# Performance work log

Measured on AMD Instinct MI355X. Metric: run time of the kernel, lower is better.

The kernel has to match this reference:

```python
import jax, jax.numpy as jnp
import numpy as np

N_NODES = 100000
N_EDGES = 1600000
N_GRAPHS = 64
IN_DIM = 128
HIDDEN = 64
OUT_DIM = 6


def gcn_conv(x, W, b, src, dst, n_nodes):
    """PyG GCNConv: D^{-1/2} (A + I) D^{-1/2} X W + b (self-loops added)."""
    xw = x @ W  # [N, H]
    # degree including self-loop (computed over destination nodes)
    deg = jax.ops.segment_sum(jnp.ones((src.shape[0],), xw.dtype), dst,
                              num_segments=n_nodes) + 1.0
    dinv = jax.lax.rsqrt(deg)  # deg >= 1, always safe
    # per-edge normalized messages, scatter-add into destinations
    coef = (dinv[src] * dinv[dst])[:, None]  # [E, 1]
    agg = jax.ops.segment_sum(xw[src] * coef, dst, num_segments=n_nodes)
    # self-loop contribution: dinv[i]^2 * xw[i]
    agg = agg + xw * (dinv * dinv)[:, None]
    return agg + b


def setup_inputs() -> dict:
    key = jax.random.key(0)
    ks = jax.random.split(key, 9)
    x = jax.random.normal(ks[0], (N_NODES, IN_DIM), dtype=jnp.float32)
    edge_index = jax.random.randint(ks[1], (2, N_EDGES), 0, N_NODES, dtype=jnp.int64)
    batch = jnp.sort(jax.random.randint(ks[2], (N_NODES,), 0, N_GRAPHS, dtype=jnp.int64))
    # Glorot-ish params
    W1 = jax.random.normal(ks[3], (IN_DIM, HIDDEN), dtype=jnp.float32) / np.sqrt(IN_DIM)
    b1 = jnp.zeros((HIDDEN,), jnp.float32)
    W2 = jax.random.normal(ks[4], (HIDDEN, HIDDEN), dtype=jnp.float32) / np.sqrt(HIDDEN)
    b2 = jnp.zeros((HIDDEN,), jnp.float32)
    Wl = jax.random.normal(ks[5], (HIDDEN, OUT_DIM), dtype=jnp.float32) / np.sqrt(HIDDEN)
    bl = jnp.zeros((OUT_DIM,), jnp.float32)
    return {"x": x, "edge_index": edge_index, "batch": batch,
            "W1": W1, "b1": b1, "W2": W2, "b2": b2, "Wl": Wl, "bl": bl}


def reference(x, edge_index, batch, W1, b1, W2, b2, Wl, bl):
    src, dst = edge_index[0], edge_index[1]
    h = jax.nn.relu(gcn_conv(x, W1, b1, src, dst, N_NODES))
    # dropout is identity in eval mode
    h = gcn_conv(h, W2, b2, src, dst, N_NODES)
    # global mean pool over graph ids
    sums = jax.ops.segment_sum(h, batch, num_segments=N_GRAPHS)  # [G, H]
    cnts = jax.ops.segment_sum(jnp.ones((h.shape[0],), h.dtype), batch,
                               num_segments=N_GRAPHS)
    pooled = sums / jnp.maximum(cnts, 1.0)[:, None]
    return pooled @ Wl + bl  # [G, OUT_DIM]
```

## Files before the change

kernel.cpp:

```cpp
#include <hip/hip_runtime.h>

#define NCOL 64
#define BSH 8
#define NBMAX 512
#define EPB 2048
#define P2CAP 6144
#define NREP 8

typedef __attribute__((ext_vector_type(8))) short bf16x8;
typedef __attribute__((ext_vector_type(4))) float f32x4;


__device__ __forceinline__ float bf_lo(unsigned int v) { return __uint_as_float(v << 16); }
__device__ __forceinline__ float bf_hi(unsigned int v) { return __uint_as_float(v & 0xFFFF0000u); }
__device__ __forceinline__ unsigned short bfs(float x) {
  unsigned int u = __float_as_uint(x);
  u = (u + 0x7FFFu + ((u >> 16) & 1u)) >> 16;
  return (unsigned short)u;
}


__global__ __launch_bounds__(256) void bin_p1(const int* __restrict__ src,
                                              const int* __restrict__ dst,
                                              unsigned int* __restrict__ ent,
                                              int* __restrict__ blockOff,
                                              int ne, int nb) {
  __shared__ int hist[NBMAX];
  __shared__ int base[NBMAX];
  __shared__ int part[256];
  __shared__ unsigned int stage[EPB];
  int tid = threadIdx.x;
  int e0 = blockIdx.x * EPB;
  int cnt = min(EPB, ne - e0);

  for (int i = tid; i < NBMAX; i += 256) hist[i] = 0;
  __syncthreads();
  for (int i = tid; i < cnt; i += 256) {
    int d = dst[e0 + i];
    atomicAdd(&hist[d >> BSH], 1);
  }
  __syncthreads();

  int a0 = hist[2 * tid], a1 = hist[2 * tid + 1];
  int s = a0 + a1;
  part[tid] = s;
  __syncthreads();
  for (int d = 1; d < 256; d <<= 1) {
    int v = (tid >= d) ? part[tid - d] : 0;
    __syncthreads();
    part[tid] += v;
    __syncthreads();
  }
  int off = part[tid] - s;
  base[2 * tid] = off;
  base[2 * tid + 1] = off + a0;
  __syncthreads();

  for (int b = tid; b < nb; b += 256) blockOff[(size_t)blockIdx.x * nb + b] = base[b];
  for (int i = tid; i < NBMAX; i += 256) hist[i] = base[i];
  __syncthreads();

  for (int i = tid; i < cnt; i += 256) {
    int d = dst[e0 + i];
    int sv = src[e0 + i];
    unsigned int e = ((unsigned int)(d & ((1 << BSH) - 1)) << 17) | (unsigned int)sv;
    int p = atomicAdd(&hist[d >> BSH], 1);
    stage[p] = e;
  }
  __syncthreads();
  for (int i = tid; i < cnt; i += 256) ent[e0 + i] = stage[i];
}


__global__ __launch_bounds__(256) void deg_bin(const unsigned int* __restrict__ ent,
                                               const int* __restrict__ blockOff,
                                               int* __restrict__ degi,
                                               int n, int ne, int nb, int nblk) {
  __shared__ int cnt[256];
  int b = blockIdx.x;
  int tid = threadIdx.x;
  cnt[tid] = 0;
  __syncthreads();
  for (int blk = tid; blk < nblk; blk += 256) {
    int e0 = blk * EPB;
    int bcnt = min(EPB, ne - e0);
    int st = blockOff[(size_t)blk * nb + b];
    int en = (b + 1 < nb) ? blockOff[(size_t)blk * nb + b + 1] : bcnt;
    for (int i = st; i < en; ++i) {
      unsigned int e = ent[e0 + i];
      atomicAdd(&cnt[e >> 17], 1);
    }
  }
  __syncthreads();
  int node = (b << BSH) + tid;
  if (node < n) degi[node] = cnt[tid];
}

__global__ void dinv_kernel(const int* __restrict__ degi, float* __restrict__ dinv, int n) {
  int i = blockIdx.x * blockDim.x + threadIdx.x;
  if (i < n) dinv[i] = rsqrtf((float)degi[i] + 1.0f);
}


__global__ void bounds_kernel(const int* __restrict__ batch, int* __restrict__ startg,
                              int* __restrict__ endg, int n) {
  int i = blockIdx.x * blockDim.x + threadIdx.x;
  if (i >= n) return;
  int b = batch[i];
  if (i == 0) {
    startg[b] = 0;
  } else {
    int bp = batch[i - 1];
    if (b != bp) { startg[b] = i; endg[bp] = i; }
  }
  if (i == n - 1) endg[b] = n;
}


#define SCAN_C 8

__global__ void scan_part(const int* __restrict__ degi, int* __restrict__ tsum,
                          int n, int nthreads) {
  int t = blockIdx.x * blockDim.x + threadIdx.x;
  if (t >= nthreads) return;
  int lo = t * SCAN_C, hi = min(lo + SCAN_C, n);
  int s = 0;
  for (int i = lo; i < hi; ++i) s += degi[i];
  tsum[t] = s;
}

__global__ void scan_mid(int* __restrict__ tsum, int* __restrict__ toff, int nthreads) {
  __shared__ int part[1024];
  int t = threadIdx.x;
  int chunk = (nthreads + 1023) >> 10;
  int lo = t * chunk, hi = min(lo + chunk, nthreads);
  int s = 0;
  for (int i = lo; i < hi; ++i) s += tsum[i];
  part[t] = s;
  __syncthreads();
  for (int d = 1; d < 1024; d <<= 1) {
    int v = (t >= d) ? part[t - d] : 0;
    __syncthreads();
    part[t] += v;
    __syncthreads();
  }
  int off = part[t] - s;
  for (int i = lo; i < hi; ++i) { toff[i] = off; off += tsum[i]; }
}

__global__ void scan_fill(const int* __restrict__ degi, const int* __restrict__ toff,
                          int* __restrict__ rowptr, int n, int nthreads) {
  int t = blockIdx.x * blockDim.x + threadIdx.x;
  if (t >= nthreads) return;
  int lo = t * SCAN_C, hi = min(lo + SCAN_C, n);
  int off = toff[t];
  for (int i = lo; i < hi; ++i) {
    rowptr[i] = off;
    off += degi[i];
  }
  if (hi == n) rowptr[n] = off;
}


__global__ __launch_bounds__(256) void bin_p2(const unsigned int* __restrict__ ent,
                                              const int* __restrict__ blockOff,
                                              const int* __restrict__ rowptr,
                                              int* __restrict__ csr_src,
                                              int n, int ne, int nb, int nblk) {
  __shared__ int cur[256];
  __shared__ int outS[P2CAP];
  int b = blockIdx.x;
  int tid = threadIdx.x;
  int node0 = b << BSH;
  int node1 = min(node0 + 256, n);
  int bucketBase = rowptr[node0];
  int bucketCnt = rowptr[node1] - bucketBase;
  int node = node0 + tid;
  cur[tid] = (node < node1) ? (rowptr[node] - bucketBase) : 0;
  __syncthreads();
  for (int blk = tid; blk < nblk; blk += 256) {
    int e0 = blk * EPB;
    int bcnt = min(EPB, ne - e0);
    int st = blockOff[(size_t)blk * nb + b];
    int en = (b + 1 < nb) ? blockOff[(size_t)blk * nb + b + 1] : bcnt;
    for (int i = st; i < en; ++i) {
      unsigned int e = ent[e0 + i];
      int dL = e >> 17;
      int sv = (int)(e & 0x1FFFFu);
      int p = atomicAdd(&cur[dL], 1);
      if (p < P2CAP) outS[p] = sv;
      else csr_src[bucketBase + p] = sv;
    }
  }
  __syncthreads();
  int lim = min(bucketCnt, P2CAP);
  for (int i = tid; i < lim; i += 256) csr_src[bucketBase + i] = outS[i];
}


template<int K>
__global__ __launch_bounds__(256, 8) void gemm_mfma(
    const float* __restrict__ X, const float* __restrict__ W,
    const float* __restrict__ dinv, unsigned int* __restrict__ Ybf, int n) {
  __shared__ unsigned short YS[64][64];
  int tid = threadIdx.x;
  int w = tid >> 6;
  int l = tid & 63;
  int lr = l & 15;
  int lk = l >> 4;
  int rows0 = blockIdx.x * 64;

  bf16x8 bfrag[K / 32];
#pragma unroll
  for (int s = 0; s < K / 32; ++s) {
#pragma unroll
    for (int j = 0; j < 8; ++j) {
      int k = s * 32 + lk * 8 + j;
      bfrag[s][j] = (short)bfs(W[(size_t)k * NCOL + 16 * w + lr]);
    }
  }

  f32x4 acc[4];
#pragma unroll
  for (int rt = 0; rt < 4; ++rt) acc[rt] = (f32x4){0.f, 0.f, 0.f, 0.f};

#pragma unroll
  for (int rt = 0; rt < 4; ++rt) {
    int row = min(rows0 + rt * 16 + lr, n - 1);
    const float* xr = X + (size_t)row * K + lk * 8;
#pragma unroll
    for (int s = 0; s < K / 32; ++s) {
      float4 x0 = *reinterpret_cast<const float4*>(xr + s * 32);
      float4 x1 = *reinterpret_cast<const float4*>(xr + s * 32 + 4);
      bf16x8 af;
      af[0] = (short)bfs(x0.x); af[1] = (short)bfs(x0.y);
      af[2] = (short)bfs(x0.z); af[3] = (short)bfs(x0.w);
      af[4] = (short)bfs(x1.x); af[5] = (short)bfs(x1.y);
      af[6] = (short)bfs(x1.z); af[7] = (short)bfs(x1.w);
      acc[rt] = __builtin_amdgcn_mfma_f32_16x16x32_bf16(af, bfrag[s], acc[rt], 0, 0, 0);
    }
  }

#pragma unroll
  for (int rt = 0; rt < 4; ++rt) {
#pragma unroll
    for (int j = 0; j < 4; ++j) {
      int row = rt * 16 + lk * 4 + j;
      float d = dinv[min(rows0 + row, n - 1)];
      YS[row][16 * w + lr] = bfs(acc[rt][j] * d);
    }
  }
  __syncthreads();

  const uint4* ys4 = reinterpret_cast<const uint4*>(&YS[0][0]);
  for (int idx = tid; idx < 512; idx += 256) {
    int row = idx >> 3;
    int gr = rows0 + row;
    if (gr < n)
      reinterpret_cast<uint4*>(Ybf + (size_t)gr * 32)[idx & 7] = ys4[idx];
  }
}


__global__ __launch_bounds__(256) void aggregate_relu(
    const int* __restrict__ rowptr, const int* __restrict__ csr_src,
    const uint4* __restrict__ Ybf4, const float* __restrict__ dinv,
    const float* __restrict__ bias, float* __restrict__ H, int n) {
  int nd = (blockIdx.x * blockDim.x + threadIdx.x) >> 3;
  if (nd >= n) return;
  int l = threadIdx.x & 7;
  int lo = rowptr[nd], hi = rowptr[nd + 1];

  uint4 vs = Ybf4[(size_t)nd * 8 + l];
  float a0 = bf_lo(vs.x), a1 = bf_hi(vs.x);
  float a2 = bf_lo(vs.y), a3 = bf_hi(vs.y);
  float a4 = bf_lo(vs.z), a5 = bf_hi(vs.z);
  float a6 = bf_lo(vs.w), a7 = bf_hi(vs.w);

  int p = lo;
  for (; p + 3 < hi; p += 4) {
    int s0 = csr_src[p];
    int s1 = csr_src[p + 1];
    int s2 = csr_src[p + 2];
    int s3 = csr_src[p + 3];
    uint4 v0 = Ybf4[(size_t)s0 * 8 + l];
    uint4 v1 = Ybf4[(size_t)s1 * 8 + l];
    uint4 v2 = Ybf4[(size_t)s2 * 8 + l];
    uint4 v3 = Ybf4[(size_t)s3 * 8 + l];
    a0 += bf_lo(v0.x); a1 += bf_hi(v0.x);
    a2 += bf_lo(v0.y); a3 += bf_hi(v0.y);
    a4 += bf_lo(v0.z); a5 += bf_hi(v0.z);
    a6 += bf_lo(v0.w); a7 += bf_hi(v0.w);
    a0 += bf_lo(v1.x); a1 += bf_hi(v1.x);
    a2 += bf_lo(v1.y); a3 += bf_hi(v1.y);
    a4 += bf_lo(v1.z); a5 += bf_hi(v1.z);
    a6 += bf_lo(v1.w); a7 += bf_hi(v1.w);
    a0 += bf_lo(v2.x); a1 += bf_hi(v2.x);
    a2 += bf_lo(v2.y); a3 += bf_hi(v2.y);
    a4 += bf_lo(v2.z); a5 += bf_hi(v2.z);
    a6 += bf_lo(v2.w); a7 += bf_hi(v2.w);
    a0 += bf_lo(v3.x); a1 += bf_hi(v3.x);
    a2 += bf_lo(v3.y); a3 += bf_hi(v3.y);
    a4 += bf_lo(v3.z); a5 += bf_hi(v3.z);
    a6 += bf_lo(v3.w); a7 += bf_hi(v3.w);
  }
  for (; p < hi; ++p) {
    int s = csr_src[p];
    uint4 v = Ybf4[(size_t)s * 8 + l];
    a0 += bf_lo(v.x); a1 += bf_hi(v.x);
    a2 += bf_lo(v.y); a3 += bf_hi(v.y);
    a4 += bf_lo(v.z); a5 += bf_hi(v.z);
    a6 += bf_lo(v.w); a7 += bf_hi(v.w);
  }

  float d = dinv[nd];
  float4 b0 = *reinterpret_cast<const float4*>(bias + l * 8);
  float4 b1 = *reinterpret_cast<const float4*>(bias + l * 8 + 4);
  float4 o0, o1;
  o0.x = fmaf(d, a0, b0.x); o0.y = fmaf(d, a1, b0.y);
  o0.z = fmaf(d, a2, b0.z); o0.w = fmaf(d, a3, b0.w);
  o1.x = fmaf(d, a4, b1.x); o1.y = fmaf(d, a5, b1.y);
  o1.z = fmaf(d, a6, b1.z); o1.w = fmaf(d, a7, b1.w);
  o0.x = fmaxf(o0.x, 0.f); o0.y = fmaxf(o0.y, 0.f);
  o0.z = fmaxf(o0.z, 0.f); o0.w = fmaxf(o0.w, 0.f);
  o1.x = fmaxf(o1.x, 0.f); o1.y = fmaxf(o1.y, 0.f);
  o1.z = fmaxf(o1.z, 0.f); o1.w = fmaxf(o1.w, 0.f);
  float* hr = H + (size_t)nd * NCOL + l * 8;
  *reinterpret_cast<float4*>(hr) = o0;
  *reinterpret_cast<float4*>(hr + 4) = o1;
}


__global__ __launch_bounds__(256) void aggregate_pool(
    const int* __restrict__ rowptr, const int* __restrict__ csr_src,
    const uint4* __restrict__ Ybf4, const float* __restrict__ dinv,
    const float* __restrict__ bias, const int* __restrict__ batch,
    float* __restrict__ poolrep, int n) {
  __shared__ float poolS[4][64];
  __shared__ int gS[4];
  __shared__ int uniS[4];
  int tid = threadIdx.x;
  int nd = (blockIdx.x * blockDim.x + tid) >> 3;
  int w = tid >> 6;
  int l = tid & 7;
  bool active = nd < n;
  int ndc = active ? nd : (n - 1);
  int lo = rowptr[ndc];
  int hi = active ? rowptr[ndc + 1] : lo;

  uint4 vs = Ybf4[(size_t)ndc * 8 + l];
  float a0 = bf_lo(vs.x), a1 = bf_hi(vs.x);
  float a2 = bf_lo(vs.y), a3 = bf_hi(vs.y);
  float a4 = bf_lo(vs.z), a5 = bf_hi(vs.z);
  float a6 = bf_lo(vs.w), a7 = bf_hi(vs.w);

  int p = lo;
  for (; p + 3 < hi; p += 4) {
    int s0 = csr_src[p];
    int s1 = csr_src[p + 1];
    int s2 = csr_src[p + 2];
    int s3 = csr_src[p + 3];
    uint4 v0 = Ybf4[(size_t)s0 * 8 + l];
    uint4 v1 = Ybf4[(size_t)s1 * 8 + l];
    uint4 v2 = Ybf4[(size_t)s2 * 8 + l];
    uint4 v3 = Ybf4[(size_t)s3 * 8 + l];
    a0 += bf_lo(v0.x); a1 += bf_hi(v0.x);
    a2 += bf_lo(v0.y); a3 += bf_hi(v0.y);
    a4 += bf_lo(v0.z); a5 += bf_hi(v0.z);
    a6 += bf_lo(v0.w); a7 += bf_hi(v0.w);
    a0 += bf_lo(v1.x); a1 += bf_hi(v1.x);
    a2 += bf_lo(v1.y); a3 += bf_hi(v1.y);
    a4 += bf_lo(v1.z); a5 += bf_hi(v1.z);
    a6 += bf_lo(v1.w); a7 += bf_hi(v1.w);
    a0 += bf_lo(v2.x); a1 += bf_hi(v2.x);
    a2 += bf_lo(v2.y); a3 += bf_hi(v2.y);
    a4 += bf_lo(v2.z); a5 += bf_hi(v2.z);
    a6 += bf_lo(v2.w); a7 += bf_hi(v2.w);
    a0 += bf_lo(v3.x); a1 += bf_hi(v3.x);
    a2 += bf_lo(v3.y); a3 += bf_hi(v3.y);
    a4 += bf_lo(v3.z); a5 += bf_hi(v3.z);
    a6 += bf_lo(v3.w); a7 += bf_hi(v3.w);
  }
  for (; p < hi; ++p) {
    int s = csr_src[p];
    uint4 v = Ybf4[(size_t)s * 8 + l];
    a0 += bf_lo(v.x); a1 += bf_hi(v.x);
    a2 += bf_lo(v.y); a3 += bf_hi(v.y);
    a4 += bf_lo(v.z); a5 += bf_hi(v.z);
    a6 += bf_lo(v.w); a7 += bf_hi(v.w);
  }

  float d = dinv[ndc];
  float4 b0 = *reinterpret_cast<const float4*>(bias + l * 8);
  float4 b1 = *reinterpret_cast<const float4*>(bias + l * 8 + 4);
  float4 o0, o1;
  o0.x = fmaf(d, a0, b0.x); o0.y = fmaf(d, a1, b0.y);
  o0.z = fmaf(d, a2, b0.z); o0.w = fmaf(d, a3, b0.w);
  o1.x = fmaf(d, a4, b1.x); o1.y = fmaf(d, a5, b1.y);
  o1.z = fmaf(d, a6, b1.z); o1.w = fmaf(d, a7, b1.w);

  float* rep = poolrep + (size_t)(blockIdx.x & (NREP - 1)) * 4096;
  int gg = active ? batch[nd] : -1;
  int waveFirstNd = (blockIdx.x * blockDim.x + (tid & ~63)) >> 3;
  bool full = (waveFirstNd + 8 <= n);
  int g0 = __builtin_amdgcn_readfirstlane(gg);
  bool uni = full && __all(gg == g0);

  if (uni) {
#pragma unroll
    for (int m = 8; m < 64; m <<= 1) {
      o0.x += __shfl_xor(o0.x, m); o0.y += __shfl_xor(o0.y, m);
      o0.z += __shfl_xor(o0.z, m); o0.w += __shfl_xor(o0.w, m);
      o1.x += __shfl_xor(o1.x, m); o1.y += __shfl_xor(o1.y, m);
      o1.z += __shfl_xor(o1.z, m); o1.w += __shfl_xor(o1.w, m);
    }
    if ((tid & 63) < 8) {
      *reinterpret_cast<float4*>(&poolS[w][l * 8]) = o0;
      *reinterpret_cast<float4*>(&poolS[w][l * 8 + 4]) = o1;
    }
    if ((tid & 63) == 0) { gS[w] = g0; uniS[w] = 1; }
  } else {
    if ((tid & 63) == 0) { gS[w] = -1; uniS[w] = 0; }
    if (active) {
      float* pr = rep + (size_t)gg * NCOL + l * 8;
      atomicAdd(pr + 0, o0.x); atomicAdd(pr + 1, o0.y);
      atomicAdd(pr + 2, o0.z); atomicAdd(pr + 3, o0.w);
      atomicAdd(pr + 4, o1.x); atomicAdd(pr + 5, o1.y);
      atomicAdd(pr + 6, o1.z); atomicAdd(pr + 7, o1.w);
    }
  }
  __syncthreads();

  if (tid < 64) {
    bool bu = uniS[0] && uniS[1] && uniS[2] && uniS[3] &&
              gS[0] == gS[1] && gS[1] == gS[2] && gS[2] == gS[3];
    if (bu) {
      float s = poolS[0][tid] + poolS[1][tid] + poolS[2][tid] + poolS[3][tid];
      atomicAdd(&rep[(size_t)gS[0] * NCOL + tid], s);
    } else {
#pragma unroll
      for (int ww = 0; ww < 4; ++ww)
        if (uniS[ww]) atomicAdd(&rep[(size_t)gS[ww] * NCOL + tid], poolS[ww][tid]);
    }
  }
}


__global__ void final_kernel(const float* __restrict__ poolrep,
                             const int* __restrict__ startg,
                             const int* __restrict__ endg, const float* __restrict__ Wl,
                             const float* __restrict__ bl, float* __restrict__ out, int ng) {
  __shared__ float poolL[4096];
  int t = threadIdx.x;
  for (int idx = t; idx < ng * NCOL; idx += blockDim.x) {
    float s = 0.f;
#pragma unroll
    for (int r = 0; r < NREP; ++r) s += poolrep[(size_t)r * 4096 + idx];
    poolL[idx] = s;
  }
  __syncthreads();
  if (t >= ng * 6) return;
  int g = t / 6, o = t % 6;
  float cntf = (float)(endg[g] - startg[g]);
  float inv = 1.0f / fmaxf(cntf, 1.0f);
  float s = 0.f;
#pragma unroll
  for (int c = 0; c < NCOL; ++c) s += poolL[g * NCOL + c] * Wl[c * 6 + o];
  out[t] = fmaf(s, inv, bl[o]);
}


extern "C" void kernel_launch(void* const* d_in, const int* in_sizes, int n_in,
                              void* d_out, int out_size, void* d_ws, size_t ws_size,
                              hipStream_t stream) {
  const float* x    = (const float*)d_in[0];
  const int*   ei   = (const int*)d_in[1];
  const int*   batch= (const int*)d_in[2];
  const float* W1   = (const float*)d_in[3];
  const float* b1   = (const float*)d_in[4];
  const float* W2   = (const float*)d_in[5];
  const float* b2   = (const float*)d_in[6];
  const float* Wl   = (const float*)d_in[7];
  const float* bl   = (const float*)d_in[8];
  float* out = (float*)d_out;

  int n  = in_sizes[0] / 128;
  int ne = in_sizes[1] / 2;
  int ng = out_size / 6;
  const int* srcI = ei;
  const int* dstI = ei + ne;

  int nb   = (n + 255) >> BSH;
  int nblk = (ne + EPB - 1) / EPB;

  char* w = (char*)d_ws;
  size_t o = 0;
  auto take = [&](size_t bytes) -> char* {
    char* p = w + o;
    o = (o + bytes + 255) & ~(size_t)255;
    return p;
  };
  float*        dinv    = (float*)take((size_t)n * 4);
  int*          degi    = (int*)  take((size_t)n * 4);
  int*          rowptr  = (int*)  take((size_t)(n + 1) * 4);
  int*          csr_src = (int*)  take((size_t)ne * 4);
  unsigned int* ent     = (unsigned int*)take((size_t)ne * 4);
  int*          blockOff= (int*)  take((size_t)nblk * nb * 4);
  unsigned int* Ybf     = (unsigned int*)take((size_t)n * (NCOL / 2) * 4);
  float*        H       = (float*)take((size_t)n * NCOL * 4);
  float*        poolrep = (float*)take((size_t)NREP * 4096 * 4);
  int*          startg  = (int*)  take(64 * 4);
  int*          endg    = (int*)  take(64 * 4);
  int*          tsum    = (int*)  take(16384 * 4);
  int*          toff    = (int*)  take(16384 * 4);

  hipMemsetAsync(poolrep, 0, (size_t)NREP * 4096 * 4, stream);
  hipMemsetAsync(startg, 0, 64 * 4, stream);
  hipMemsetAsync(endg, 0, 64 * 4, stream);

  int nb256 = (n + 255) / 256;
  int nthreads = (n + SCAN_C - 1) / SCAN_C;
  int nbScan = (nthreads + 255) / 256;

  bin_p1<<<nblk, 256, 0, stream>>>(srcI, dstI, ent, blockOff, ne, nb);
  deg_bin<<<nb, 256, 0, stream>>>(ent, blockOff, degi, n, ne, nb, nblk);
  bounds_kernel<<<nb256, 256, 0, stream>>>(batch, startg, endg, n);
  dinv_kernel<<<nb256, 256, 0, stream>>>(degi, dinv, n);
  scan_part<<<nbScan, 256, 0, stream>>>(degi, tsum, n, nthreads);
  scan_mid<<<1, 1024, 0, stream>>>(tsum, toff, nthreads);
  scan_fill<<<nbScan, 256, 0, stream>>>(degi, toff, rowptr, n, nthreads);
  bin_p2<<<nb, 256, 0, stream>>>(ent, blockOff, rowptr, csr_src, n, ne, nb, nblk);

  int nbAgg = (n * 8 + 255) / 256;
  int nbGemm = (n + 63) / 64;

  gemm_mfma<128><<<nbGemm, 256, 0, stream>>>(x, W1, dinv, Ybf, n);
  aggregate_relu<<<nbAgg, 256, 0, stream>>>(rowptr, csr_src, (const uint4*)Ybf,
                                            dinv, b1, H, n);

  gemm_mfma<64><<<nbGemm, 256, 0, stream>>>(H, W2, dinv, Ybf, n);
  aggregate_pool<<<nbAgg, 256, 0, stream>>>(rowptr, csr_src, (const uint4*)Ybf,
                                            dinv, b2, batch, poolrep, n);

  final_kernel<<<1, 384, 0, stream>>>(poolrep, startg, endg, Wl, bl, out, ng);
}
```

Measured before the change: 211.9 us.

## Globally sort edge entries by destination bucket before degree and CSR passes

Replaces the per-block local binning with a global two-pass counting sort: a histogram kernel, a bucket-major prefix scan over (bucket, block) counts, then a scatter that writes each block's bucket slices to global sorted offsets. Degree counting and CSR fill then read one contiguous range per bucket with all threads striding over it, instead of each thread serially walking a per-block slice. This is meant to remove the uncoalesced, load-imbalanced per-thread serial loops in deg_bin/bin_p2. In exchange it adds an extra pass over dst, three scan kernels with integer divisions, and a scatter whose per-bucket copy loop is serial per thread and poorly coalesced.

```diff
diff --git a/kernel.cpp b/kernel.cpp
--- a/kernel.cpp
+++ b/kernel.cpp
@@ -6,6 +6,8 @@
 #define EPB 2048
 #define P2CAP 6144
 #define NREP 8
+#define SCAN_C 8
+#define SCAN2_C 16
 
 typedef __attribute__((ext_vector_type(8))) short bf16x8;
 typedef __attribute__((ext_vector_type(4))) float f32x4;
@@ -20,25 +22,86 @@
 }
 
 
-__global__ __launch_bounds__(256) void bin_p1(const int* __restrict__ src,
-                                              const int* __restrict__ dst,
-                                              unsigned int* __restrict__ ent,
-                                              int* __restrict__ blockOff,
-                                              int ne, int nb) {
+__global__ __launch_bounds__(256) void hist_p1(const int* __restrict__ dst,
+                                               int* __restrict__ blockOffC,
+                                               int ne, int nb) {
+  __shared__ int hist[NBMAX];
+  int tid = threadIdx.x;
+  int e0 = blockIdx.x * EPB;
+  int cnt = min(EPB, ne - e0);
+  for (int i = tid; i < NBMAX; i += 256) hist[i] = 0;
+  __syncthreads();
+  for (int i = tid; i < cnt; i += 256) atomicAdd(&hist[dst[e0 + i] >> BSH], 1);
+  __syncthreads();
+  for (int b = tid; b < nb; b += 256) blockOffC[(size_t)blockIdx.x * nb + b] = hist[b];
+}
+
+
+__global__ void scan2_part(const int* __restrict__ blockOffC, int* __restrict__ tsum,
+                           int total, int nthreads, int nblk, int nb) {
+  int t = blockIdx.x * blockDim.x + threadIdx.x;
+  if (t >= nthreads) return;
+  int lo = t * SCAN2_C, hi = min(lo + SCAN2_C, total);
+  int s = 0;
+  for (int f = lo; f < hi; ++f) {
+    int b = f / nblk, blk = f - b * nblk;
+    s += blockOffC[(size_t)blk * nb + b];
+  }
+  tsum[t] = s;
+}
+
+__global__ void scan_mid(int* __restrict__ tsum, int* __restrict__ toff, int nthreads) {
+  __shared__ int part[1024];
+  int t = threadIdx.x;
+  int chunk = (nthreads + 1023) >> 10;
+  int lo = t * chunk, hi = min(lo + chunk, nthreads);
+  int s = 0;
+  for (int i = lo; i < hi; ++i) s += tsum[i];
+  part[t] = s;
+  __syncthreads();
+  for (int d = 1; d < 1024; d <<= 1) {
+    int v = (t >= d) ? part[t - d] : 0;
+    __syncthreads();
+    part[t] += v;
+    __syncthreads();
+  }
+  int off = part[t] - s;
+  for (int i = lo; i < hi; ++i) { toff[i] = off; off += tsum[i]; }
+}
+
+__global__ void scan2_fill(const int* __restrict__ blockOffC, const int* __restrict__ toff,
+                           int* __restrict__ sortOff, int total, int nthreads,
+                           int nblk, int nb) {
+  int t = blockIdx.x * blockDim.x + threadIdx.x;
+  if (t >= nthreads) return;
+  int lo = t * SCAN2_C, hi = min(lo + SCAN2_C, total);
+  int off = toff[t];
+  for (int f = lo; f < hi; ++f) {
+    int b = f / nblk, blk = f - b * nblk;
+    sortOff[f] = off;
+    off += blockOffC[(size_t)blk * nb + b];
+  }
+}
+
+
+__global__ __launch_bounds__(256) void scatter_p1(const int* __restrict__ src,
+                                                  const int* __restrict__ dst,
+                                                  const int* __restrict__ sortOff,
+                                                  unsigned int* __restrict__ ent,
+                                                  int ne, int nb, int nblk) {
   __shared__ int hist[NBMAX];
   __shared__ int base[NBMAX];
+  __shared__ int cntL[NBMAX];
   __shared__ int part[256];
   __shared__ unsigned int stage[EPB];
   int tid = threadIdx.x;
-  int e0 = blockIdx.x * EPB;
+  int blk = blockIdx.x;
+  int e0 = blk * EPB;
   int cnt = min(EPB, ne - e0);
 
   for (int i = tid; i < NBMAX; i += 256) hist[i] = 0;
   __syncthreads();
-  for (int i = tid; i < cnt; i += 256) {
-    int d = dst[e0 + i];
-    atomicAdd(&hist[d >> BSH], 1);
-  }
+  for (int i = tid; i < cnt; i += 256) atomicAdd(&hist[dst[e0 + i] >> BSH], 1);
   __syncthreads();
 
   int a0 = hist[2 * tid], a1 = hist[2 * tid + 1];
@@ -52,11 +115,9 @@
     __syncthreads();
   }
   int off = part[tid] - s;
-  base[2 * tid] = off;
-  base[2 * tid + 1] = off + a0;
-  __syncthreads();
-
-  for (int b = tid; b < nb; b += 256) blockOff[(size_t)blockIdx.x * nb + b] = base[b];
+  base[2 * tid] = off;      cntL[2 * tid] = a0;
+  base[2 * tid + 1] = off + a0; cntL[2 * tid + 1] = a1;
+  __syncthreads();
   for (int i = tid; i < NBMAX; i += 256) hist[i] = base[i];
   __syncthreads();
 
@@ -68,29 +129,29 @@
     stage[p] = e;
   }
   __syncthreads();
-  for (int i = tid; i < cnt; i += 256) ent[e0 + i] = stage[i];
-}
-
-
-__global__ __launch_bounds__(256) void deg_bin(const unsigned int* __restrict__ ent,
-                                               const int* __restrict__ blockOff,
-                                               int* __restrict__ degi,
-                                               int n, int ne, int nb, int nblk) {
+
+  for (int b = tid; b < nb; b += 256) {
+    int c = cntL[b];
+    if (!c) continue;
+    int s0 = base[b];
+    int d0 = sortOff[(size_t)b * nblk + blk];
+    for (int i = 0; i < c; ++i) ent[d0 + i] = stage[s0 + i];
+  }
+}
+
+
+__global__ __launch_bounds__(256) void deg_sorted(const unsigned int* __restrict__ ent,
+                                                  const int* __restrict__ sortOff,
+                                                  int* __restrict__ degi,
+                                                  int n, int ne, int nb, int nblk) {
   __shared__ int cnt[256];
   int b = blockIdx.x;
   int tid = threadIdx.x;
   cnt[tid] = 0;
   __syncthreads();
-  for (int blk = tid; blk < nblk; blk += 256) {
-    int e0 = blk * EPB;
-    int bcnt = min(EPB, ne - e0);
-    int st = blockOff[(size_t)blk * nb + b];
-    int en = (b + 1 < nb) ? blockOff[(size_t)blk * nb + b + 1] : bcnt;
-    for (int i = st; i < en; ++i) {
-      unsigned int e = ent[e0 + i];
-      atomicAdd(&cnt[e >> 17], 1);
-    }
-  }
+  int st = sortOff[(size_t)b * nblk];
+  int en = (b + 1 < nb) ? sortOff[(size_t)(b + 1) * nblk] : ne;
+  for (int i = st + tid; i < en; i += 256) atomicAdd(&cnt[ent[i] >> 17], 1);
   __syncthreads();
   int node = (b << BSH) + tid;
   if (node < n) degi[node] = cnt[tid];
@@ -117,8 +178,6 @@
 }
 
 
-#define SCAN_C 8
-
 __global__ void scan_part(const int* __restrict__ degi, int* __restrict__ tsum,
                           int n, int nthreads) {
   int t = blockIdx.x * blockDim.x + threadIdx.x;
@@ -127,25 +186,6 @@
   int s = 0;
   for (int i = lo; i < hi; ++i) s += degi[i];
   tsum[t] = s;
-}
-
-__global__ void scan_mid(int* __restrict__ tsum, int* __restrict__ toff, int nthreads) {
-  __shared__ int part[1024];
-  int t = threadIdx.x;
-  int chunk = (nthreads + 1023) >> 10;
-  int lo = t * chunk, hi = min(lo + chunk, nthreads);
-  int s = 0;
-  for (int i = lo; i < hi; ++i) s += tsum[i];
-  part[t] = s;
-  __syncthreads();
-  for (int d = 1; d < 1024; d <<= 1) {
-    int v = (t >= d) ? part[t - d] : 0;
-    __syncthreads();
-    part[t] += v;
-    __syncthreads();
-  }
-  int off = part[t] - s;
-  for (int i = lo; i < hi; ++i) { toff[i] = off; off += tsum[i]; }
 }
 
 __global__ void scan_fill(const int* __restrict__ degi, const int* __restrict__ toff,
@@ -162,11 +202,11 @@
 }
 
 
-__global__ __launch_bounds__(256) void bin_p2(const unsigned int* __restrict__ ent,
-                                              const int* __restrict__ blockOff,
-                                              const int* __restrict__ rowptr,
-                                              int* __restrict__ csr_src,
-                                              int n, int ne, int nb, int nblk) {
+__global__ __launch_bounds__(256) void p2_sorted(const unsigned int* __restrict__ ent,
+                                                 const int* __restrict__ sortOff,
+                                                 const int* __restrict__ rowptr,
+                                                 int* __restrict__ csr_src,
+                                                 int n, int ne, int nb, int nblk) {
   __shared__ int cur[256];
   __shared__ int outS[P2CAP];
   int b = blockIdx.x;
@@ -178,19 +218,15 @@
   int node = node0 + tid;
   cur[tid] = (node < node1) ? (rowptr[node] - bucketBase) : 0;
   __syncthreads();
-  for (int blk = tid; blk < nblk; blk += 256) {
-    int e0 = blk * EPB;
-    int bcnt = min(EPB, ne - e0);
-    int st = blockOff[(size_t)blk * nb + b];
-    int en = (b + 1 < nb) ? blockOff[(size_t)blk * nb + b + 1] : bcnt;
-    for (int i = st; i < en; ++i) {
-      unsigned int e = ent[e0 + i];
-      int dL = e >> 17;
-      int sv = (int)(e & 0x1FFFFu);
-      int p = atomicAdd(&cur[dL], 1);
-      if (p < P2CAP) outS[p] = sv;
-      else csr_src[bucketBase + p] = sv;
-    }
+  int st = sortOff[(size_t)b * nblk];
+  int en = (b + 1 < nb) ? sortOff[(size_t)(b + 1) * nblk] : ne;
+  for (int i = st + tid; i < en; i += 256) {
+    unsigned int e = ent[i];
+    int dL = e >> 17;
+    int sv = (int)(e & 0x1FFFFu);
+    int p = atomicAdd(&cur[dL], 1);
+    if (p < P2CAP) outS[p] = sv;
+    else csr_src[bucketBase + p] = sv;
   }
   __syncthreads();
   int lim = min(bucketCnt, P2CAP);
@@ -492,6 +528,7 @@
 
   int nb   = (n + 255) >> BSH;
   int nblk = (ne + EPB - 1) / EPB;
+  int total2 = nb * nblk;
 
   char* w = (char*)d_ws;
   size_t o = 0;
@@ -500,19 +537,20 @@
     o = (o + bytes + 255) & ~(size_t)255;
     return p;
   };
-  float*        dinv    = (float*)take((size_t)n * 4);
-  int*          degi    = (int*)  take((size_t)n * 4);
-  int*          rowptr  = (int*)  take((size_t)(n + 1) * 4);
-  int*          csr_src = (int*)  take((size_t)ne * 4);
-  unsigned int* ent     = (unsigned int*)take((size_t)ne * 4);
-  int*          blockOff= (int*)  take((size_t)nblk * nb * 4);
-  unsigned int* Ybf     = (unsigned int*)take((size_t)n * (NCOL / 2) * 4);
-  float*        H       = (float*)take((size_t)n * NCOL * 4);
-  float*        poolrep = (float*)take((size_t)NREP * 4096 * 4);
-  int*          startg  = (int*)  take(64 * 4);
-  int*          endg    = (int*)  take(64 * 4);
-  int*          tsum    = (int*)  take(16384 * 4);
-  int*          toff    = (int*)  take(16384 * 4);
+  float*        dinv     = (float*)take((size_t)n * 4);
+  int*          degi     = (int*)  take((size_t)n * 4);
+  int*          rowptr   = (int*)  take((size_t)(n + 1) * 4);
+  int*          csr_src  = (int*)  take((size_t)ne * 4);
+  unsigned int* ent      = (unsigned int*)take((size_t)ne * 4);
+  int*          blockOffC= (int*)  take((size_t)total2 * 4);
+  int*          sortOff  = (int*)  take((size_t)total2 * 4);
+  unsigned int* Ybf      = (unsigned int*)take((size_t)n * (NCOL / 2) * 4);
+  float*        H        = (float*)take((size_t)n * NCOL * 4);
+  float*        poolrep  = (float*)take((size_t)NREP * 4096 * 4);
+  int*          startg   = (int*)  take(64 * 4);
+  int*          endg     = (int*)  take(64 * 4);
+  int*          tsum     = (int*)  take(32768 * 4);
+  int*          toff     = (int*)  take(32768 * 4);
 
   hipMemsetAsync(poolrep, 0, (size_t)NREP * 4096 * 4, stream);
   hipMemsetAsync(startg, 0, 64 * 4, stream);
@@ -521,15 +559,21 @@
   int nb256 = (n + 255) / 256;
   int nthreads = (n + SCAN_C - 1) / SCAN_C;
   int nbScan = (nthreads + 255) / 256;
-
-  bin_p1<<<nblk, 256, 0, stream>>>(srcI, dstI, ent, blockOff, ne, nb);
-  deg_bin<<<nb, 256, 0, stream>>>(ent, blockOff, degi, n, ne, nb, nblk);
+  int nthreads2 = (total2 + SCAN2_C - 1) / SCAN2_C;
+  int nbScan2 = (nthreads2 + 255) / 256;
+
+  hist_p1<<<nblk, 256, 0, stream>>>(dstI, blockOffC, ne, nb);
+  scan2_part<<<nbScan2, 256, 0, stream>>>(blockOffC, tsum, total2, nthreads2, nblk, nb);
+  scan_mid<<<1, 1024, 0, stream>>>(tsum, toff, nthreads2);
+  scan2_fill<<<nbScan2, 256, 0, stream>>>(blockOffC, toff, sortOff, total2, nthreads2, nblk, nb);
+  scatter_p1<<<nblk, 256, 0, stream>>>(srcI, dstI, sortOff, ent, ne, nb, nblk);
+  deg_sorted<<<nb, 256, 0, stream>>>(ent, sortOff, degi, n, ne, nb, nblk);
   bounds_kernel<<<nb256, 256, 0, stream>>>(batch, startg, endg, n);
   dinv_kernel<<<nb256, 256, 0, stream>>>(degi, dinv, n);
   scan_part<<<nbScan, 256, 0, stream>>>(degi, tsum, n, nthreads);
   scan_mid<<<1, 1024, 0, stream>>>(tsum, toff, nthreads);
   scan_fill<<<nbScan, 256, 0, stream>>>(degi, toff, rowptr, n, nthreads);
-  bin_p2<<<nb, 256, 0, stream>>>(ent, blockOff, rowptr, csr_src, n, ne, nb, nblk);
+  p2_sorted<<<nb, 256, 0, stream>>>(ent, sortOff, rowptr, csr_src, n, ne, nb, nblk);
 
   int nbAgg = (n * 8 + 255) / 256;
   int nbGemm = (n + 63) / 64;
```

New measurement: 228.8 us. 8.0% more time.
